# Kernel tuning notes

Measured on AMD Instinct MI355X. Metric: run time of the kernel, lower is better.

Reference implementation:

```python
import jax, jax.numpy as jnp
import numpy as np
from jax import lax
from jax.scipy.special import logsumexp

S, B, H, T = 512, 128, 512, 48  # seq_len, batch, hidden_dim, tagset_size


def setup_inputs() -> dict:
    key = jax.random.key(0)
    k1, k2, k3, k4 = jax.random.split(key, 4)
    word_features = jax.random.normal(k1, (S, B, H), dtype=jnp.float32)
    W = jax.random.normal(k2, (T, H), dtype=jnp.float32) * 0.02  # linear_layer weight
    b = jnp.zeros((T,), dtype=jnp.float32)                        # linear_layer bias
    transitions = jax.random.normal(k3, (T, T), dtype=jnp.float32) * 0.01
    tags = jax.random.randint(k4, (S, B), 0, T, dtype=jnp.int32)
    return {"word_features": word_features, "W": W, "b": b,
            "transitions": transitions, "tags": tags}


def reference(word_features, W, b, transitions, tags):
    # CRFScore: emissions[s,b,t] = Linear(word_features); crf_scores[s,b,i,j] = emissions[s,b,j] + transitions[i,j]
    emissions = jnp.einsum('sbh,th->sbt', word_features, W) + b  # [S,B,T]

    # Forward algorithm (partition function) via serial logsumexp scan over time.
    def step(alpha, emit_t):
        # alpha: [B,T] log-scores ending at tag i; expand over to-tag j
        new_alpha = logsumexp(alpha[:, :, None] + transitions[None, :, :], axis=1) + emit_t
        return new_alpha, None

    alpha0 = emissions[0]                       # [B,T]
    alphaT, _ = lax.scan(step, alpha0, emissions[1:])
    log_Z = logsumexp(alphaT, axis=1)           # [B]

    # Gold path score: sum of gold emissions + gold transitions
    em_gold = jnp.take_along_axis(emissions, tags[:, :, None], axis=2)[..., 0].sum(axis=0)  # [B]
    tr_gold = transitions[tags[:-1], tags[1:]].sum(axis=0)                                   # [B]
    gold_score = em_gold + tr_gold

    # Negative log-likelihood averaged over batch
    nll = jnp.mean(log_Z - gold_score)
    return nll
```

## Files before the change

### kernel.cpp

```cpp
#include <hip/hip_runtime.h>
#include <math.h>

#define S_DIM 512
#define B_DIM 128
#define H_DIM 512
#define T_DIM 48

typedef short bf16x8 __attribute__((ext_vector_type(8)));
typedef short s16x4  __attribute__((ext_vector_type(4)));
typedef float f32x4  __attribute__((ext_vector_type(4)));

__device__ __forceinline__ short rne_bf(float f) {
  unsigned u = __float_as_uint(f);
  u += 0x7fffu + ((u >> 16) & 1u);
  return (short)(u >> 16);
}
__device__ __forceinline__ short trunc_bf(float f) {
  return (short)(__float_as_uint(f) >> 16);
}

struct Frags6 { bf16x8 b[2][3]; };

__device__ __forceinline__ void load_child(const short* __restrict__ p, int h, int q, Frags6& f) {
  bf16x8 z = 0;
#pragma unroll
  for (int ct = 0; ct < 3; ++ct) {
    const short* col = p + (16 * ct + q) * 48;
    f.b[0][ct] = *(const bf16x8*)(col + 8 * h);
    f.b[1][ct] = (h < 2) ? *(const bf16x8*)(col + 32 + 8 * h) : z;
  }
}

__device__ __forceinline__ void matstep(const short* Ml, bool useI, int h, int q,
                                        const Frags6& B, f32x4 C[3][3]) {
#pragma unroll
  for (int rt = 0; rt < 3; ++rt) {
    const int row = 16 * rt + q;
    bf16x8 a0, a1;
    if (useI) {
      const short one = (short)0x3F80;
#pragma unroll
      for (int i = 0; i < 8; ++i) {
        a0[i] = (row == 8 * h + i) ? one : (short)0;
        a1[i] = (row == 32 + 8 * h + i) ? one : (short)0;
      }
    } else {
      const int sw = (row & 7) << 3;
      a0 = *(const bf16x8*)&Ml[row * 64 + ((8 * h) ^ sw)];
      a1 = *(const bf16x8*)&Ml[row * 64 + ((32 + 8 * h) ^ sw)];
    }
#pragma unroll
    for (int ct = 0; ct < 3; ++ct) {
      C[rt][ct] = __builtin_amdgcn_mfma_f32_16x16x32_bf16(a0, B.b[0][ct], C[rt][ct], 0, 0, 0);
      C[rt][ct] = __builtin_amdgcn_mfma_f32_16x16x32_bf16(a1, B.b[1][ct], C[rt][ct], 0, 0, 0);
    }
  }
}

__device__ __forceinline__ void writeM(short* Ml, int h, int q, const f32x4 C[3][3]) {
#pragma unroll
  for (int rt = 0; rt < 3; ++rt)
#pragma unroll
    for (int ct = 0; ct < 3; ++ct) {
      const int j = 16 * ct + q;
#pragma unroll
      for (int r = 0; r < 4; ++r) {
        const int row = 16 * rt + 4 * h + r;
        Ml[row * 64 + (j ^ ((row & 7) << 3))] = trunc_bf(C[rt][ct][r]);
      }
    }
}

__device__ __forceinline__ int store_node(short* __restrict__ node, int h, int q,
                                          const f32x4 C[3][3]) {
  float mx = 0.f;
#pragma unroll
  for (int rt = 0; rt < 3; ++rt)
#pragma unroll
    for (int ct = 0; ct < 3; ++ct)
#pragma unroll
      for (int r = 0; r < 4; ++r) mx = fmaxf(mx, C[rt][ct][r]);
#pragma unroll
  for (int off = 1; off < 64; off <<= 1) mx = fmaxf(mx, __shfl_xor(mx, off, 64));
  int ex;
  frexpf(mx, &ex);
  const float sc = ldexpf(1.0f, -ex);
#pragma unroll
  for (int rt = 0; rt < 3; ++rt)
#pragma unroll
    for (int ct = 0; ct < 3; ++ct) {
      s16x4 pk;
#pragma unroll
      for (int r = 0; r < 4; ++r) pk[r] = rne_bf(C[rt][ct][r] * sc);
      *(s16x4*)&node[(16 * ct + q) * 48 + 16 * rt + 4 * h] = pk;
    }
  return ex;
}

__device__ __forceinline__ void zero_lds(short* Ml, int l) {
  s16x4 z = 0;
#pragma unroll
  for (int i = 0; i < 12; ++i) *(s16x4*)&Ml[(l + 64 * i) * 4] = z;
}

__global__ void k_prep(const float* __restrict__ W, const float* __restrict__ trans,
                       short* __restrict__ Wbf, short* __restrict__ expTcm,
                       float* __restrict__ out) {
  int idx = blockIdx.x * 256 + threadIdx.x;
  if (idx == 0) out[0] = 0.f;
  for (int i = idx; i < T_DIM * H_DIM; i += gridDim.x * 256) Wbf[i] = rne_bf(W[i]);
  for (int i = idx; i < T_DIM * T_DIM; i += gridDim.x * 256) {
    int j = i / 48, k = i - j * 48;
    expTcm[j * 48 + k] = rne_bf(__expf(trans[k * 48 + j]));
  }
}

__global__ __launch_bounds__(256) void k_emissions(
    const float* __restrict__ wf, const short* __restrict__ Wbf,
    const float* __restrict__ bias, float* __restrict__ em) {
  __shared__ short A[128 * 32];
  const int tid = threadIdx.x;
  const int w = tid >> 6, l = tid & 63, h = l >> 4, q = l & 15;
  const int r0 = blockIdx.x * 128;
  const int trow = tid >> 3, tc4 = tid & 7;

  f32x4 C[2][3];
#pragma unroll
  for (int rt = 0; rt < 2; ++rt)
#pragma unroll
    for (int ct = 0; ct < 3; ++ct) C[rt][ct] = 0.f;

  for (int ks = 0; ks < 16; ++ks) {
    const int k0 = ks * 32;
    __syncthreads();
#pragma unroll
    for (int qq = 0; qq < 4; ++qq) {
      const int row = trow + 32 * qq;
      float4 v = *(const float4*)&wf[(size_t)(r0 + row) * H_DIM + k0 + 4 * tc4];
      s16x4 pk;
      pk[0] = rne_bf(v.x); pk[1] = rne_bf(v.y); pk[2] = rne_bf(v.z); pk[3] = rne_bf(v.w);
      *(s16x4*)&A[row * 32 + ((4 * tc4) ^ ((row & 3) << 3))] = pk;
    }
    __syncthreads();
    bf16x8 bfr[3];
#pragma unroll
    for (int ct = 0; ct < 3; ++ct)
      bfr[ct] = *(const bf16x8*)&Wbf[(size_t)(16 * ct + q) * H_DIM + k0 + 8 * h];
#pragma unroll
    for (int rt = 0; rt < 2; ++rt) {
      const int row = 32 * w + 16 * rt + q;
      bf16x8 a = *(const bf16x8*)&A[row * 32 + ((8 * h) ^ ((row & 3) << 3))];
#pragma unroll
      for (int ct = 0; ct < 3; ++ct)
        C[rt][ct] = __builtin_amdgcn_mfma_f32_16x16x32_bf16(a, bfr[ct], C[rt][ct], 0, 0, 0);
    }
  }
  float bb[3];
#pragma unroll
  for (int ct = 0; ct < 3; ++ct) bb[ct] = bias[16 * ct + q];
#pragma unroll
  for (int rt = 0; rt < 2; ++rt)
#pragma unroll
    for (int ct = 0; ct < 3; ++ct)
#pragma unroll
      for (int r = 0; r < 4; ++r) {
        const int row = r0 + 32 * w + 16 * rt + 4 * h + r;
        em[(size_t)row * T_DIM + 16 * ct + q] = C[rt][ct][r] + bb[ct];
      }
}

__global__ __launch_bounds__(64) void k_tree1(
    const float* __restrict__ em, const short* __restrict__ expTcm,
    short* __restrict__ nodes1, int* __restrict__ exp1) {
  const int b = blockIdx.x >> 5, c = blockIdx.x & 31;
  const int l = threadIdx.x, h = l >> 4, q = l & 15;
  __shared__ short Ml[48 * 64];
  zero_lds(Ml, l);

  Frags6 B;
  load_child(expTcm, h, q, B);

  const int s0 = 1 + 16 * c;
  const int NT = min(16, 511 - 16 * c);
  size_t ro = (size_t)(s0 * B_DIM + b) * T_DIM;
  float eA0 = em[ro + q], eA1 = em[ro + 16 + q], eA2 = em[ro + 32 + q];
  float eB0 = 0.f, eB1 = 0.f, eB2 = 0.f;

  f32x4 C[3][3];
  for (int t = 0; t < NT; ++t) {
    if (t + 1 < NT) {
      size_t rn = (size_t)((s0 + t + 1) * B_DIM + b) * T_DIM;
      eB0 = em[rn + q]; eB1 = em[rn + 16 + q]; eB2 = em[rn + 32 + q];
    }
#pragma unroll
    for (int rt = 0; rt < 3; ++rt)
#pragma unroll
      for (int ct = 0; ct < 3; ++ct) C[rt][ct] = 0.f;
    matstep(Ml, t == 0, h, q, B, C);
    const float e0 = __expf(eA0), e1 = __expf(eA1), e2 = __expf(eA2);
#pragma unroll
    for (int rt = 0; rt < 3; ++rt)
#pragma unroll
      for (int r = 0; r < 4; ++r) {
        C[rt][0][r] *= e0; C[rt][1][r] *= e1; C[rt][2][r] *= e2;
      }
    writeM(Ml, h, q, C);
    eA0 = eB0; eA1 = eB1; eA2 = eB2;
  }
  int ex = store_node(nodes1 + (size_t)(b * 32 + c) * 2304, h, q, C);
  if (l == 0) exp1[b * 32 + c] = ex;
}

__global__ __launch_bounds__(64) void k_tree2(
    const short* __restrict__ nodes1, const int* __restrict__ exp1,
    short* __restrict__ nodes2, int* __restrict__ exp2) {
  const int b = blockIdx.x >> 2, c2 = blockIdx.x & 3;
  const int l = threadIdx.x, h = l >> 4, q = l & 15;
  __shared__ short Ml[48 * 64];
  zero_lds(Ml, l);

  const short* base = nodes1 + (size_t)(b * 32 + 8 * c2) * 2304;
  Frags6 B, Bn;
  load_child(base, h, q, B);
  f32x4 C[3][3];
  for (int t = 0; t < 8; ++t) {
    if (t < 7) load_child(base + (size_t)(t + 1) * 2304, h, q, Bn);
#pragma unroll
    for (int rt = 0; rt < 3; ++rt)
#pragma unroll
      for (int ct = 0; ct < 3; ++ct) C[rt][ct] = 0.f;
    matstep(Ml, t == 0, h, q, B, C);
    if (t < 7) { writeM(Ml, h, q, C); B = Bn; }
  }
  int ex = store_node(nodes2 + (size_t)(b * 4 + c2) * 2304, h, q, C);
  int ce = (l < 8) ? exp1[b * 32 + 8 * c2 + l] : 0;
  ce += __shfl_xor(ce, 1, 64); ce += __shfl_xor(ce, 2, 64); ce += __shfl_xor(ce, 4, 64);
  if (l == 0) exp2[b * 4 + c2] = ex + ce;
}

__global__ __launch_bounds__(64) void k_tree3(
    const short* __restrict__ nodes2, const int* __restrict__ exp2,
    const float* __restrict__ em, const float* __restrict__ trans,
    const int* __restrict__ tags, float* __restrict__ out) {
  const int b = blockIdx.x;
  const int l = threadIdx.x, h = l >> 4, q = l & 15;
  __shared__ short Ml[48 * 64];
  zero_lds(Ml, l);

  const short* base = nodes2 + (size_t)(b * 4) * 2304;
  Frags6 B, Bn;
  load_child(base, h, q, B);
  f32x4 C[3][3];
  for (int t = 0; t < 4; ++t) {
    if (t < 3) load_child(base + (size_t)(t + 1) * 2304, h, q, Bn);
#pragma unroll
    for (int rt = 0; rt < 3; ++rt)
#pragma unroll
      for (int ct = 0; ct < 3; ++ct) C[rt][ct] = 0.f;
    matstep(Ml, t == 0, h, q, B, C);
    if (t < 3) { writeM(Ml, h, q, C); B = Bn; }
  }
  float Zp = 0.f;
#pragma unroll
  for (int rt = 0; rt < 3; ++rt)
#pragma unroll
    for (int r = 0; r < 4; ++r) {
      float rs = C[rt][0][r] + C[rt][1][r] + C[rt][2][r];
      rs += __shfl_xor(rs, 1, 64); rs += __shfl_xor(rs, 2, 64);
      rs += __shfl_xor(rs, 4, 64); rs += __shfl_xor(rs, 8, 64);
      const int row = 16 * rt + 4 * h + r;
      Zp = fmaf(__expf(em[(size_t)b * T_DIM + row]), rs, Zp);
    }
  Zp += __shfl_xor(Zp, 16, 64); Zp += __shfl_xor(Zp, 32, 64);
  int E = (l < 4) ? exp2[b * 4 + l] : 0;
  E += __shfl_xor(E, 1, 64); E += __shfl_xor(E, 2, 64);
  const float logZ = __logf(Zp) + (float)E * 0.69314718055994531f;

  float g = 0.f;
  for (int s = l; s < S_DIM; s += 64) {
    const int tg = tags[s * B_DIM + b];
    g += em[(size_t)(s * B_DIM + b) * T_DIM + tg];
    if (s < S_DIM - 1) {
      const int tn = tags[(s + 1) * B_DIM + b];
      g += trans[tg * T_DIM + tn];
    }
  }
#pragma unroll
  for (int off = 1; off < 64; off <<= 1) g += __shfl_xor(g, off, 64);
  if (l == 0) atomicAdd(out, (logZ - g) * (1.0f / (float)B_DIM));
}

extern "C" void kernel_launch(void* const* d_in, const int* in_sizes, int n_in,
                              void* d_out, int out_size, void* d_ws, size_t ws_size,
                              hipStream_t stream) {
  const float* wf    = (const float*)d_in[0];
  const float* W     = (const float*)d_in[1];
  const float* bias  = (const float*)d_in[2];
  const float* trans = (const float*)d_in[3];
  const int*   tags  = (const int*)d_in[4];
  float* out = (float*)d_out;

  char* p = (char*)d_ws;
  float* em     = (float*)p;            p += (size_t)S_DIM * B_DIM * T_DIM * 4;
  short* nodes1 = (short*)p;            p += (size_t)128 * 32 * 2304 * 2;
  short* nodes2 = (short*)p;            p += (size_t)128 * 4 * 2304 * 2;
  short* Wbf    = (short*)p;            p += (size_t)T_DIM * H_DIM * 2;
  short* expTcm = (short*)p;            p += (size_t)48 * 48 * 2 + 32;
  int*   exp1   = (int*)p;              p += 128 * 32 * 4;
  int*   exp2   = (int*)p;

  k_prep<<<32, 256, 0, stream>>>(W, trans, Wbf, expTcm, out);
  k_emissions<<<512, 256, 0, stream>>>(wf, Wbf, bias, em);
  k_tree1<<<128 * 32, 64, 0, stream>>>(em, expTcm, nodes1, exp1);
  k_tree2<<<128 * 4, 64, 0, stream>>>(nodes1, exp1, nodes2, exp2);
  k_tree3<<<128, 64, 0, stream>>>(nodes2, exp2, em, trans, tags, out);
}
```

Baseline: 256.4 us.

## Fuse prep and tree reduction kernels into fewer launches

Removes the prep kernel by converting W and exp(transitions) to bf16 inline inside the emissions and tree1 kernels. The emissions GEMM now loads operands straight from global memory into registers, dropping the LDS staging and its barriers. tree2 and tree3 are merged into one 256-thread final kernel that reduces 8 children per wave, combines the four results in LDS and overlaps the gold-path sum. Cutting from five launches to three removes launch gaps and the nodes2 round trip, at the cost of redundant conversions and uncoalesced W reads in each block.

```diff
diff --git a/kernel.cpp b/kernel.cpp
--- a/kernel.cpp
+++ b/kernel.cpp
@@ -18,6 +18,13 @@
 __device__ __forceinline__ short trunc_bf(float f) {
   return (short)(__float_as_uint(f) >> 16);
 }
+__device__ __forceinline__ bf16x8 cvt8(const float* __restrict__ p) {
+  float4 v0 = *(const float4*)p, v1 = *(const float4*)(p + 4);
+  bf16x8 r;
+  r[0] = rne_bf(v0.x); r[1] = rne_bf(v0.y); r[2] = rne_bf(v0.z); r[3] = rne_bf(v0.w);
+  r[4] = rne_bf(v1.x); r[5] = rne_bf(v1.y); r[6] = rne_bf(v1.z); r[7] = rne_bf(v1.w);
+  return r;
+}
 
 struct Frags6 { bf16x8 b[2][3]; };
 
@@ -33,6 +40,7 @@
 
 __device__ __forceinline__ void matstep(const short* Ml, bool useI, int h, int q,
                                         const Frags6& B, f32x4 C[3][3]) {
+  const f32x4 Z = {0.f, 0.f, 0.f, 0.f};
 #pragma unroll
   for (int rt = 0; rt < 3; ++rt) {
     const int row = 16 * rt + q;
@@ -50,10 +58,10 @@
       a1 = *(const bf16x8*)&Ml[row * 64 + ((32 + 8 * h) ^ sw)];
     }
 #pragma unroll
-    for (int ct = 0; ct < 3; ++ct) {
-      C[rt][ct] = __builtin_amdgcn_mfma_f32_16x16x32_bf16(a0, B.b[0][ct], C[rt][ct], 0, 0, 0);
-      C[rt][ct] = __builtin_amdgcn_mfma_f32_16x16x32_bf16(a1, B.b[1][ct], C[rt][ct], 0, 0, 0);
-    }
+    for (int ct = 0; ct < 3; ++ct)
+      C[rt][ct] = __builtin_amdgcn_mfma_f32_16x16x32_bf16(
+          a1, B.b[1][ct],
+          __builtin_amdgcn_mfma_f32_16x16x32_bf16(a0, B.b[0][ct], Z, 0, 0, 0), 0, 0, 0);
   }
 }
 
@@ -71,8 +79,20 @@
     }
 }
 
-__device__ __forceinline__ int store_node(short* __restrict__ node, int h, int q,
-                                          const f32x4 C[3][3]) {
+__device__ __forceinline__ void storecol(short* __restrict__ node, int h, int q,
+                                         const f32x4 C[3][3]) {
+#pragma unroll
+  for (int rt = 0; rt < 3; ++rt)
+#pragma unroll
+    for (int ct = 0; ct < 3; ++ct) {
+      s16x4 pk;
+#pragma unroll
+      for (int r = 0; r < 4; ++r) pk[r] = rne_bf(C[rt][ct][r]);
+      *(s16x4*)&node[(16 * ct + q) * 48 + 16 * rt + 4 * h] = pk;
+    }
+}
+
+__device__ __forceinline__ int rescaleC(f32x4 C[3][3]) {
   float mx = 0.f;
 #pragma unroll
   for (int rt = 0; rt < 3; ++rt)
@@ -88,12 +108,16 @@
 #pragma unroll
   for (int rt = 0; rt < 3; ++rt)
 #pragma unroll
-    for (int ct = 0; ct < 3; ++ct) {
-      s16x4 pk;
-#pragma unroll
-      for (int r = 0; r < 4; ++r) pk[r] = rne_bf(C[rt][ct][r] * sc);
-      *(s16x4*)&node[(16 * ct + q) * 48 + 16 * rt + 4 * h] = pk;
-    }
+    for (int ct = 0; ct < 3; ++ct)
+#pragma unroll
+      for (int r = 0; r < 4; ++r) C[rt][ct][r] *= sc;
+  return ex;
+}
+
+__device__ __forceinline__ int store_node(short* __restrict__ node, int h, int q,
+                                          f32x4 C[3][3]) {
+  int ex = rescaleC(C);
+  storecol(node, h, q, C);
   return ex;
 }
 
@@ -103,26 +127,14 @@
   for (int i = 0; i < 12; ++i) *(s16x4*)&Ml[(l + 64 * i) * 4] = z;
 }
 
-__global__ void k_prep(const float* __restrict__ W, const float* __restrict__ trans,
-                       short* __restrict__ Wbf, short* __restrict__ expTcm,
-                       float* __restrict__ out) {
-  int idx = blockIdx.x * 256 + threadIdx.x;
-  if (idx == 0) out[0] = 0.f;
-  for (int i = idx; i < T_DIM * H_DIM; i += gridDim.x * 256) Wbf[i] = rne_bf(W[i]);
-  for (int i = idx; i < T_DIM * T_DIM; i += gridDim.x * 256) {
-    int j = i / 48, k = i - j * 48;
-    expTcm[j * 48 + k] = rne_bf(__expf(trans[k * 48 + j]));
-  }
-}
-
 __global__ __launch_bounds__(256) void k_emissions(
-    const float* __restrict__ wf, const short* __restrict__ Wbf,
-    const float* __restrict__ bias, float* __restrict__ em) {
-  __shared__ short A[128 * 32];
+    const float* __restrict__ wf, const float* __restrict__ W,
+    const float* __restrict__ bias, float* __restrict__ em,
+    float* __restrict__ out) {
+  if (blockIdx.x == 0 && threadIdx.x == 0) out[0] = 0.0f;
   const int tid = threadIdx.x;
   const int w = tid >> 6, l = tid & 63, h = l >> 4, q = l & 15;
-  const int r0 = blockIdx.x * 128;
-  const int trow = tid >> 3, tc4 = tid & 7;
+  const size_t r0 = (size_t)blockIdx.x * 128;
 
   f32x4 C[2][3];
 #pragma unroll
@@ -131,46 +143,36 @@
     for (int ct = 0; ct < 3; ++ct) C[rt][ct] = 0.f;
 
   for (int ks = 0; ks < 16; ++ks) {
-    const int k0 = ks * 32;
-    __syncthreads();
-#pragma unroll
-    for (int qq = 0; qq < 4; ++qq) {
-      const int row = trow + 32 * qq;
-      float4 v = *(const float4*)&wf[(size_t)(r0 + row) * H_DIM + k0 + 4 * tc4];
-      s16x4 pk;
-      pk[0] = rne_bf(v.x); pk[1] = rne_bf(v.y); pk[2] = rne_bf(v.z); pk[3] = rne_bf(v.w);
-      *(s16x4*)&A[row * 32 + ((4 * tc4) ^ ((row & 3) << 3))] = pk;
-    }
-    __syncthreads();
-    bf16x8 bfr[3];
-#pragma unroll
-    for (int ct = 0; ct < 3; ++ct)
-      bfr[ct] = *(const bf16x8*)&Wbf[(size_t)(16 * ct + q) * H_DIM + k0 + 8 * h];
-#pragma unroll
-    for (int rt = 0; rt < 2; ++rt) {
-      const int row = 32 * w + 16 * rt + q;
-      bf16x8 a = *(const bf16x8*)&A[row * 32 + ((8 * h) ^ ((row & 3) << 3))];
+    const int k0 = 32 * ks + 8 * h;
+    bf16x8 a[2], bb[3];
+#pragma unroll
+    for (int rt = 0; rt < 2; ++rt)
+      a[rt] = cvt8(&wf[(r0 + 32 * w + 16 * rt + q) * H_DIM + k0]);
+#pragma unroll
+    for (int ct = 0; ct < 3; ++ct)
+      bb[ct] = cvt8(&W[(size_t)(16 * ct + q) * H_DIM + k0]);
+#pragma unroll
+    for (int rt = 0; rt < 2; ++rt)
 #pragma unroll
       for (int ct = 0; ct < 3; ++ct)
-        C[rt][ct] = __builtin_amdgcn_mfma_f32_16x16x32_bf16(a, bfr[ct], C[rt][ct], 0, 0, 0);
-    }
-  }
-  float bb[3];
-#pragma unroll
-  for (int ct = 0; ct < 3; ++ct) bb[ct] = bias[16 * ct + q];
+        C[rt][ct] = __builtin_amdgcn_mfma_f32_16x16x32_bf16(a[rt], bb[ct], C[rt][ct], 0, 0, 0);
+  }
+  float bv[3];
+#pragma unroll
+  for (int ct = 0; ct < 3; ++ct) bv[ct] = bias[16 * ct + q];
 #pragma unroll
   for (int rt = 0; rt < 2; ++rt)
 #pragma unroll
     for (int ct = 0; ct < 3; ++ct)
 #pragma unroll
       for (int r = 0; r < 4; ++r) {
-        const int row = r0 + 32 * w + 16 * rt + 4 * h + r;
-        em[(size_t)row * T_DIM + 16 * ct + q] = C[rt][ct][r] + bb[ct];
+        const size_t row = r0 + 32 * w + 16 * rt + 4 * h + r;
+        em[row * T_DIM + 16 * ct + q] = C[rt][ct][r] + bv[ct];
       }
 }
 
 __global__ __launch_bounds__(64) void k_tree1(
-    const float* __restrict__ em, const short* __restrict__ expTcm,
+    const float* __restrict__ em, const float* __restrict__ trans,
     short* __restrict__ nodes1, int* __restrict__ exp1) {
   const int b = blockIdx.x >> 5, c = blockIdx.x & 31;
   const int l = threadIdx.x, h = l >> 4, q = l & 15;
@@ -178,31 +180,36 @@
   zero_lds(Ml, l);
 
   Frags6 B;
-  load_child(expTcm, h, q, B);
+#pragma unroll
+  for (int ct = 0; ct < 3; ++ct) {
+    const int j = 16 * ct + q;
+#pragma unroll
+    for (int i = 0; i < 8; ++i) {
+      const int k0 = 8 * h + i;
+      B.b[0][ct][i] = rne_bf(__expf(trans[k0 * T_DIM + j]));
+      const int k1 = 32 + 8 * h + i;
+      B.b[1][ct][i] = (k1 < T_DIM) ? rne_bf(__expf(trans[k1 * T_DIM + j])) : (short)0;
+    }
+  }
 
   const int s0 = 1 + 16 * c;
   const int NT = min(16, 511 - 16 * c);
   size_t ro = (size_t)(s0 * B_DIM + b) * T_DIM;
-  float eA0 = em[ro + q], eA1 = em[ro + 16 + q], eA2 = em[ro + 32 + q];
+  float eA0 = __expf(em[ro + q]), eA1 = __expf(em[ro + 16 + q]), eA2 = __expf(em[ro + 32 + q]);
   float eB0 = 0.f, eB1 = 0.f, eB2 = 0.f;
 
   f32x4 C[3][3];
   for (int t = 0; t < NT; ++t) {
     if (t + 1 < NT) {
       size_t rn = (size_t)((s0 + t + 1) * B_DIM + b) * T_DIM;
-      eB0 = em[rn + q]; eB1 = em[rn + 16 + q]; eB2 = em[rn + 32 + q];
-    }
+      eB0 = __expf(em[rn + q]); eB1 = __expf(em[rn + 16 + q]); eB2 = __expf(em[rn + 32 + q]);
+    }
+    matstep(Ml, t == 0, h, q, B, C);
 #pragma unroll
     for (int rt = 0; rt < 3; ++rt)
 #pragma unroll
-      for (int ct = 0; ct < 3; ++ct) C[rt][ct] = 0.f;
-    matstep(Ml, t == 0, h, q, B, C);
-    const float e0 = __expf(eA0), e1 = __expf(eA1), e2 = __expf(eA2);
-#pragma unroll
-    for (int rt = 0; rt < 3; ++rt)
-#pragma unroll
       for (int r = 0; r < 4; ++r) {
-        C[rt][0][r] *= e0; C[rt][1][r] *= e1; C[rt][2][r] *= e2;
+        C[rt][0][r] *= eA0; C[rt][1][r] *= eA1; C[rt][2][r] *= eA2;
       }
     writeM(Ml, h, q, C);
     eA0 = eB0; eA1 = eB1; eA2 = eB2;
@@ -211,83 +218,69 @@
   if (l == 0) exp1[b * 32 + c] = ex;
 }
 
-__global__ __launch_bounds__(64) void k_tree2(
+__global__ __launch_bounds__(256) void k_final(
     const short* __restrict__ nodes1, const int* __restrict__ exp1,
-    short* __restrict__ nodes2, int* __restrict__ exp2) {
-  const int b = blockIdx.x >> 2, c2 = blockIdx.x & 3;
-  const int l = threadIdx.x, h = l >> 4, q = l & 15;
-  __shared__ short Ml[48 * 64];
-  zero_lds(Ml, l);
-
-  const short* base = nodes1 + (size_t)(b * 32 + 8 * c2) * 2304;
+    const float* __restrict__ em, const float* __restrict__ trans,
+    const int* __restrict__ tags, float* __restrict__ out) {
+  const int b = blockIdx.x, tid = threadIdx.x;
+  const int v = tid >> 6, l = tid & 63, h = l >> 4, q = l & 15;
+  __shared__ short Ml[4][48 * 64];
+  __shared__ short Pc[3][2304];
+  __shared__ float gred[4];
+  __shared__ int wexp[4];
+
+  float g = 0.f;
+  for (int s = tid; s < S_DIM; s += 256) {
+    const int tg = tags[s * B_DIM + b];
+    g += em[(size_t)(s * B_DIM + b) * T_DIM + tg];
+    if (s < S_DIM - 1) g += trans[tg * T_DIM + tags[(s + 1) * B_DIM + b]];
+  }
+#pragma unroll
+  for (int off = 1; off < 64; off <<= 1) g += __shfl_xor(g, off, 64);
+  if (l == 0) gred[v] = g;
+
+  zero_lds(Ml[v], l);
+  const short* base = nodes1 + (size_t)(b * 32 + 8 * v) * 2304;
   Frags6 B, Bn;
   load_child(base, h, q, B);
   f32x4 C[3][3];
   for (int t = 0; t < 8; ++t) {
     if (t < 7) load_child(base + (size_t)(t + 1) * 2304, h, q, Bn);
+    matstep(Ml[v], t == 0, h, q, B, C);
+    if (t < 7) { writeM(Ml[v], h, q, C); B = Bn; }
+  }
+  int ex = rescaleC(C);
+  if (l == 0) wexp[v] = ex;
+  if (v > 0) storecol(Pc[v - 1], h, q, C);
+  else       writeM(Ml[0], h, q, C);
+  __syncthreads();
+
+  if (v == 0) {
+    for (int t = 0; t < 3; ++t) {
+      load_child(Pc[t], h, q, B);
+      matstep(Ml[0], false, h, q, B, C);
+      if (t < 2) writeM(Ml[0], h, q, C);
+    }
+    float Zp = 0.f;
 #pragma unroll
     for (int rt = 0; rt < 3; ++rt)
 #pragma unroll
-      for (int ct = 0; ct < 3; ++ct) C[rt][ct] = 0.f;
-    matstep(Ml, t == 0, h, q, B, C);
-    if (t < 7) { writeM(Ml, h, q, C); B = Bn; }
-  }
-  int ex = store_node(nodes2 + (size_t)(b * 4 + c2) * 2304, h, q, C);
-  int ce = (l < 8) ? exp1[b * 32 + 8 * c2 + l] : 0;
-  ce += __shfl_xor(ce, 1, 64); ce += __shfl_xor(ce, 2, 64); ce += __shfl_xor(ce, 4, 64);
-  if (l == 0) exp2[b * 4 + c2] = ex + ce;
-}
-
-__global__ __launch_bounds__(64) void k_tree3(
-    const short* __restrict__ nodes2, const int* __restrict__ exp2,
-    const float* __restrict__ em, const float* __restrict__ trans,
-    const int* __restrict__ tags, float* __restrict__ out) {
-  const int b = blockIdx.x;
-  const int l = threadIdx.x, h = l >> 4, q = l & 15;
-  __shared__ short Ml[48 * 64];
-  zero_lds(Ml, l);
-
-  const short* base = nodes2 + (size_t)(b * 4) * 2304;
-  Frags6 B, Bn;
-  load_child(base, h, q, B);
-  f32x4 C[3][3];
-  for (int t = 0; t < 4; ++t) {
-    if (t < 3) load_child(base + (size_t)(t + 1) * 2304, h, q, Bn);
-#pragma unroll
-    for (int rt = 0; rt < 3; ++rt)
-#pragma unroll
-      for (int ct = 0; ct < 3; ++ct) C[rt][ct] = 0.f;
-    matstep(Ml, t == 0, h, q, B, C);
-    if (t < 3) { writeM(Ml, h, q, C); B = Bn; }
-  }
-  float Zp = 0.f;
-#pragma unroll
-  for (int rt = 0; rt < 3; ++rt)
-#pragma unroll
-    for (int r = 0; r < 4; ++r) {
-      float rs = C[rt][0][r] + C[rt][1][r] + C[rt][2][r];
-      rs += __shfl_xor(rs, 1, 64); rs += __shfl_xor(rs, 2, 64);
-      rs += __shfl_xor(rs, 4, 64); rs += __shfl_xor(rs, 8, 64);
-      const int row = 16 * rt + 4 * h + r;
-      Zp = fmaf(__expf(em[(size_t)b * T_DIM + row]), rs, Zp);
-    }
-  Zp += __shfl_xor(Zp, 16, 64); Zp += __shfl_xor(Zp, 32, 64);
-  int E = (l < 4) ? exp2[b * 4 + l] : 0;
-  E += __shfl_xor(E, 1, 64); E += __shfl_xor(E, 2, 64);
-  const float logZ = __logf(Zp) + (float)E * 0.69314718055994531f;
-
-  float g = 0.f;
-  for (int s = l; s < S_DIM; s += 64) {
-    const int tg = tags[s * B_DIM + b];
-    g += em[(size_t)(s * B_DIM + b) * T_DIM + tg];
-    if (s < S_DIM - 1) {
-      const int tn = tags[(s + 1) * B_DIM + b];
-      g += trans[tg * T_DIM + tn];
-    }
-  }
-#pragma unroll
-  for (int off = 1; off < 64; off <<= 1) g += __shfl_xor(g, off, 64);
-  if (l == 0) atomicAdd(out, (logZ - g) * (1.0f / (float)B_DIM));
+      for (int r = 0; r < 4; ++r) {
+        float rs = C[rt][0][r] + C[rt][1][r] + C[rt][2][r];
+        rs += __shfl_xor(rs, 1, 64); rs += __shfl_xor(rs, 2, 64);
+        rs += __shfl_xor(rs, 4, 64); rs += __shfl_xor(rs, 8, 64);
+        const int row = 16 * rt + 4 * h + r;
+        Zp = fmaf(__expf(em[(size_t)b * T_DIM + row]), rs, Zp);
+      }
+    Zp += __shfl_xor(Zp, 16, 64); Zp += __shfl_xor(Zp, 32, 64);
+    int E = (l < 32) ? exp1[b * 32 + l] : 0;
+#pragma unroll
+    for (int off = 1; off < 32; off <<= 1) E += __shfl_xor(E, off, 64);
+    E += wexp[0] + wexp[1] + wexp[2] + wexp[3];
+    const float logZ = __logf(Zp) + (float)E * 0.69314718055994531f;
+    const float gold = gred[0] + gred[1] + gred[2] + gred[3];
+    if (l == 0) atomicAdd(out, (logZ - gold) * (1.0f / (float)B_DIM));
+  }
 }
 
 extern "C" void kernel_launch(void* const* d_in, const int* in_sizes, int n_in,
@@ -301,17 +294,11 @@
   float* out = (float*)d_out;
 
   char* p = (char*)d_ws;
-  float* em     = (float*)p;            p += (size_t)S_DIM * B_DIM * T_DIM * 4;
-  short* nodes1 = (short*)p;            p += (size_t)128 * 32 * 2304 * 2;
-  short* nodes2 = (short*)p;            p += (size_t)128 * 4 * 2304 * 2;
-  short* Wbf    = (short*)p;            p += (size_t)T_DIM * H_DIM * 2;
-  short* expTcm = (short*)p;            p += (size_t)48 * 48 * 2 + 32;
-  int*   exp1   = (int*)p;              p += 128 * 32 * 4;
-  int*   exp2   = (int*)p;
-
-  k_prep<<<32, 256, 0, stream>>>(W, trans, Wbf, expTcm, out);
-  k_emissions<<<512, 256, 0, stream>>>(wf, Wbf, bias, em);
-  k_tree1<<<128 * 32, 64, 0, stream>>>(em, expTcm, nodes1, exp1);
-  k_tree2<<<128 * 4, 64, 0, stream>>>(nodes1, exp1, nodes2, exp2);
-  k_tree3<<<128, 64, 0, stream>>>(nodes2, exp2, em, trans, tags, out);
-}
+  float* em     = (float*)p;  p += (size_t)S_DIM * B_DIM * T_DIM * 4;
+  short* nodes1 = (short*)p;  p += (size_t)128 * 32 * 2304 * 2;
+  int*   exp1   = (int*)p;
+
+  k_emissions<<<512, 256, 0, stream>>>(wf, W, bias, em, out);
+  k_tree1<<<128 * 32, 64, 0, stream>>>(em, trans, nodes1, exp1);
+  k_final<<<128, 256, 0, stream>>>(nodes1, exp1, em, trans, tags, out);
+}
```

Measured after the change: 253.8 us. No clear change (-1.0%).
